# Kernel tuning notes

Hardware: AMD Instinct MI355X
Metric: run time of the kernel (lower is better)

The kernel has to match this reference:

```python
import jax, jax.numpy as jnp
import numpy as np

EPS = 1e-5


def _create_scalars(x0, x, N, basis, v):
    # x0: [b,NT,3], x/v: [b,NT,ND,3], N: [b,NT], basis: [b,Nb,3]
    b, NT, ND, _ = x.shape
    v0 = jnp.mean(v, axis=2)                       # [b,NT,3]
    v = v - v0[:, :, None, :]
    feats = []
    # local_N normalization (log scaling)
    Nn = jnp.log1p(N.astype(x.dtype))
    feats.append(jnp.broadcast_to(Nn[:, :, None, None], (b, NT, ND, 1)))
    x0n = jnp.linalg.norm(x0, axis=-1, keepdims=True) + EPS   # [b,NT,1]
    feats.append(jnp.broadcast_to(x0n[:, :, None, :], (b, NT, ND, 1)))
    x0u = x0 / x0n
    x0b = jnp.einsum('bid,bjd->bij', x0u, basis)              # [b,NT,Nb]
    feats.append(jnp.broadcast_to(x0b[:, :, None, :], (b, NT, ND, x0b.shape[-1])))
    v0n = jnp.linalg.norm(v0, axis=-1, keepdims=True) + EPS
    feats.append(jnp.broadcast_to(v0n[:, :, None, :], (b, NT, ND, 1)))
    v0u = v0 / v0n
    v0b = jnp.einsum('bid,bjd->bij', v0u, basis)
    feats.append(jnp.broadcast_to(v0b[:, :, None, :], (b, NT, ND, v0b.shape[-1])))
    x0v0 = jnp.einsum('bid,bid->bi', x0u, v0u)                # [b,NT]
    feats.append(jnp.broadcast_to(x0v0[:, :, None, None], (b, NT, ND, 1)))
    xn = jnp.linalg.norm(x, axis=-1, keepdims=True) + EPS     # [b,NT,ND,1]
    feats.append(xn)
    xu = x / xn
    feats.append(jnp.einsum('bijd,bkd->bijk', xu, basis))     # [b,NT,ND,Nb]
    vn = jnp.linalg.norm(v, axis=-1, keepdims=True) + EPS
    feats.append(vn)
    vu = v / vn
    feats.append(jnp.einsum('bijd,bkd->bijk', vu, basis))
    feats.append(jnp.einsum('bijd,bijd->bij', xu, vu)[..., None])
    return jnp.concatenate(feats, axis=-1)                    # [b,NT,ND,19]


def setup_inputs() -> dict:
    key = jax.random.key(0)
    ks = jax.random.split(key, 12)
    b, NT, ND, Nb = 4, 1024, 128, 3
    k_in, H, L = 19, 256, 128
    s0 = 1.0 / np.sqrt(k_in)
    s1 = 1.0 / np.sqrt(H)
    return {
        'x0': jax.random.normal(ks[0], (b, NT, 3), jnp.float32),
        'x': jax.random.normal(ks[1], (b, NT, ND, 3), jnp.float32),
        'N': jax.random.randint(ks[2], (b, NT), 1, 1000),
        'basis': jax.random.normal(ks[3], (b, Nb, 3), jnp.float32),
        'v': jax.random.normal(ks[4], (b, NT, ND, 3), jnp.float32),
        'W0': jax.random.normal(ks[5], (k_in, H), jnp.float32) * s0,
        'b0': jnp.zeros((H,), jnp.float32),
        'W1': jax.random.normal(ks[6], (H, H), jnp.float32) * s1,
        'b1': jnp.zeros((H,), jnp.float32),
        'W2': jax.random.normal(ks[7], (H, L), jnp.float32) * s1,
        'b2': jnp.zeros((L,), jnp.float32),
    }


def reference(x0, x, N, basis, v, W0, b0, W1, b1, W2, b2):
    s = _create_scalars(x0, x, N, basis, v)            # [b,NT,ND,19]
    h = jax.nn.leaky_relu(s @ W0 + b0)                 # layer 0 MLP
    h = jnp.mean(h, axis=2)                            # pool over N_DM -> [b,NT,H]
    h = jax.nn.leaky_relu(h @ W1 + b1)                 # layer 1
    return h @ W2 + b2                                 # layer 2 -> [b,NT,Nlatent]
```

## Files before the change

### kernel.cpp

```cpp
#include <hip/hip_runtime.h>
#include <math.h>

#define EPSF 1e-5f
constexpr int NT  = 1024;
constexpr int ND  = 128;
constexpr int KIN = 19;
constexpr int H   = 256;
constexpr int L   = 128;

typedef __attribute__((ext_vector_type(8))) short short8;
typedef __attribute__((ext_vector_type(4))) float f32x4;

static __device__ inline unsigned cvt_pk_bf16(float lo, float hi) {
    unsigned r;
    asm("v_cvt_pk_bf16_f32 %0, %1, %2" : "=v"(r) : "v"(lo), "v"(hi));
    return r;
}

__global__ __launch_bounds__(256) void k_fused(
    const float* __restrict__ x0, const float* __restrict__ x,
    const int*   __restrict__ Nv, const float* __restrict__ basis,
    const float* __restrict__ v,  const float* __restrict__ W0,
    const float* __restrict__ b0, float* __restrict__ hm_out)
{
    const int tid  = threadIdx.x;
    const int lane = tid & 63;
    const int w    = tid >> 6;
    const int g2   = blockIdx.x * 2;

    __shared__ __align__(16) ushort featb[2 * 512 * 8];
    __shared__ float psh[2][2][3];

    {
        const int sub  = tid >> 7;
        const int d    = tid & 127;
        const int g    = g2 + sub;
        const int bidx = g >> 10;

        const float* xp = x + (size_t)g * (ND * 3);
        const float* vp = v + (size_t)g * (ND * 3);
        const float vx = vp[d*3+0], vy = vp[d*3+1], vz = vp[d*3+2];
        const float xx = xp[d*3+0], xy = xp[d*3+1], xz = xp[d*3+2];

        float sx = vx, sy = vy, sz = vz;
        #pragma unroll
        for (int m = 1; m < 64; m <<= 1) {
            sx += __shfl_xor(sx, m, 64);
            sy += __shfl_xor(sy, m, 64);
            sz += __shfl_xor(sz, m, 64);
        }
        if (lane == 0) {
            psh[sub][w & 1][0] = sx;
            psh[sub][w & 1][1] = sy;
            psh[sub][w & 1][2] = sz;
        }
        __syncthreads();
        const float invd = 1.0f / (float)ND;
        const float v0x = (psh[sub][0][0] + psh[sub][1][0]) * invd;
        const float v0y = (psh[sub][0][1] + psh[sub][1][1]) * invd;
        const float v0z = (psh[sub][0][2] + psh[sub][1][2]) * invd;

        const float* bs = basis + bidx * 9;
        const float b0c = bs[0], b1c = bs[1], b2c = bs[2];
        const float b3c = bs[3], b4c = bs[4], b5c = bs[5];
        const float b6c = bs[6], b7c = bs[7], b8c = bs[8];

        unsigned u0, u1, u2, u3, u4;
        {
            const float ax = x0[g*3+0], ay = x0[g*3+1], az = x0[g*3+2];
            const float x0n = sqrtf(ax*ax + ay*ay + az*az) + EPSF;
            const float v0n = sqrtf(v0x*v0x + v0y*v0y + v0z*v0z) + EPSF;
            const float ix  = 1.f / x0n, iv0 = 1.f / v0n;
            u0 = cvt_pk_bf16(log1pf((float)Nv[g]), x0n);
            u1 = cvt_pk_bf16((ax*b0c + ay*b1c + az*b2c) * ix,
                             (ax*b3c + ay*b4c + az*b5c) * ix);
            u2 = cvt_pk_bf16((ax*b6c + ay*b7c + az*b8c) * ix, v0n);
            u3 = cvt_pk_bf16((v0x*b0c + v0y*b1c + v0z*b2c) * iv0,
                             (v0x*b3c + v0y*b4c + v0z*b5c) * iv0);
            u4 = cvt_pk_bf16((v0x*b6c + v0y*b7c + v0z*b8c) * iv0,
                             (ax*v0x + ay*v0y + az*v0z) * ix * iv0);
        }
        unsigned u5, u6, u7, u8, u9;
        {
            const float cx = vx - v0x, cy = vy - v0y, cz = vz - v0z;
            const float xn = sqrtf(xx*xx + xy*xy + xz*xz) + EPSF;
            const float vn = sqrtf(cx*cx + cy*cy + cz*cz) + EPSF;
            const float ixn = 1.f/xn, ivn = 1.f/vn;
            u5 = cvt_pk_bf16(xn, (xx*b0c + xy*b1c + xz*b2c) * ixn);
            u6 = cvt_pk_bf16((xx*b3c + xy*b4c + xz*b5c) * ixn,
                             (xx*b6c + xy*b7c + xz*b8c) * ixn);
            u7 = cvt_pk_bf16(vn, (cx*b0c + cy*b1c + cz*b2c) * ivn);
            u8 = cvt_pk_bf16((cx*b3c + cy*b4c + cz*b5c) * ivn,
                             (cx*b6c + cy*b7c + cz*b8c) * ivn);
            u9 = cvt_pk_bf16((xx*cx + xy*cy + xz*cz) * ixn * ivn, 1.0f);
        }

        const int mt  = d >> 4;
        const int r16 = d & 15;
        uint4* base = reinterpret_cast<uint4*>(
            &featb[((sub << 9) + (mt << 6) + r16) * 8]);
        base[0]  = uint4{u0, u1, u2, u3};
        base[16] = uint4{u4, u5, u6, u7};
        base[32] = uint4{u8, u9, 0u, 0u};
        base[48] = uint4{0u, 0u, 0u, 0u};
    }
    __syncthreads();

    short8 bfrag[4];
    {
        const int col16 = lane & 15;
        const int kb    = lane >> 4;
        #pragma unroll
        for (int nt = 0; nt < 4; ++nt) {
            const int col = w * 64 + nt * 16 + col16;
            uint4 pk;
            #pragma unroll
            for (int jj = 0; jj < 4; ++jj) {
                const int k0 = kb * 8 + 2*jj;
                const int k1 = k0 + 1;
                const float a = (k0 < KIN) ? W0[k0 * H + col]
                               : ((k0 == KIN) ? b0[col] : 0.f);
                const float b = (k1 < KIN) ? W0[k1 * H + col]
                               : ((k1 == KIN) ? b0[col] : 0.f);
                (&pk.x)[jj] = cvt_pk_bf16(a, b);
            }
            bfrag[nt] = *reinterpret_cast<short8*>(&pk);
        }
    }

    const f32x4 zc = {0.f, 0.f, 0.f, 0.f};
    const float invd = 1.0f / (float)ND;

    float a00 = 0.f, a01 = 0.f, a02 = 0.f, a03 = 0.f;
    float a10 = 0.f, a11 = 0.f, a12 = 0.f, a13 = 0.f;

    #pragma unroll 2
    for (int mt = 0; mt < 8; ++mt) {
        const short8 af0 = *reinterpret_cast<const short8*>(
            &featb[((mt << 6) + lane) * 8]);
        const short8 af1 = *reinterpret_cast<const short8*>(
            &featb[((512 + (mt << 6) + lane)) * 8]);
        {
            f32x4 d0 = __builtin_amdgcn_mfma_f32_16x16x32_bf16(af0, bfrag[0], zc, 0, 0, 0);
            f32x4 d1 = __builtin_amdgcn_mfma_f32_16x16x32_bf16(af1, bfrag[0], zc, 0, 0, 0);
            #pragma unroll
            for (int r = 0; r < 4; ++r) {
                a00 = fmaf(0.505f, d0[r], fmaf(0.495f, fabsf(d0[r]), a00));
                a10 = fmaf(0.505f, d1[r], fmaf(0.495f, fabsf(d1[r]), a10));
            }
        }
        {
            f32x4 d0 = __builtin_amdgcn_mfma_f32_16x16x32_bf16(af0, bfrag[1], zc, 0, 0, 0);
            f32x4 d1 = __builtin_amdgcn_mfma_f32_16x16x32_bf16(af1, bfrag[1], zc, 0, 0, 0);
            #pragma unroll
            for (int r = 0; r < 4; ++r) {
                a01 = fmaf(0.505f, d0[r], fmaf(0.495f, fabsf(d0[r]), a01));
                a11 = fmaf(0.505f, d1[r], fmaf(0.495f, fabsf(d1[r]), a11));
            }
        }
        {
            f32x4 d0 = __builtin_amdgcn_mfma_f32_16x16x32_bf16(af0, bfrag[2], zc, 0, 0, 0);
            f32x4 d1 = __builtin_amdgcn_mfma_f32_16x16x32_bf16(af1, bfrag[2], zc, 0, 0, 0);
            #pragma unroll
            for (int r = 0; r < 4; ++r) {
                a02 = fmaf(0.505f, d0[r], fmaf(0.495f, fabsf(d0[r]), a02));
                a12 = fmaf(0.505f, d1[r], fmaf(0.495f, fabsf(d1[r]), a12));
            }
        }
        {
            f32x4 d0 = __builtin_amdgcn_mfma_f32_16x16x32_bf16(af0, bfrag[3], zc, 0, 0, 0);
            f32x4 d1 = __builtin_amdgcn_mfma_f32_16x16x32_bf16(af1, bfrag[3], zc, 0, 0, 0);
            #pragma unroll
            for (int r = 0; r < 4; ++r) {
                a03 = fmaf(0.505f, d0[r], fmaf(0.495f, fabsf(d0[r]), a03));
                a13 = fmaf(0.505f, d1[r], fmaf(0.495f, fabsf(d1[r]), a13));
            }
        }
    }

    {
        float sv0[4] = {a00, a01, a02, a03};
        float sv1[4] = {a10, a11, a12, a13};
        #pragma unroll
        for (int nt = 0; nt < 4; ++nt) {
            float s4 = sv0[nt];
            s4 += __shfl_xor(s4, 16, 64);
            s4 += __shfl_xor(s4, 32, 64);
            float s5 = sv1[nt];
            s5 += __shfl_xor(s5, 16, 64);
            s5 += __shfl_xor(s5, 32, 64);
            if (lane < 16) {
                hm_out[(size_t)(g2 + 0) * H + w * 64 + nt * 16 + lane] = s4 * invd;
                hm_out[(size_t)(g2 + 1) * H + w * 64 + nt * 16 + lane] = s5 * invd;
            }
        }
    }
}

__global__ __launch_bounds__(256) void k_l12(
    const float* __restrict__ hm, const float* __restrict__ W1,
    const float* __restrict__ b1, const float* __restrict__ W2,
    const float* __restrict__ b2, float* __restrict__ out)
{
    const int tb  = blockIdx.x * 8;
    const int tid = threadIdx.x;
    __shared__ float hs[8][H];
    __shared__ float h1[8][H];

    {
        const float4* src = reinterpret_cast<const float4*>(hm + (size_t)tb * H);
        float4* dst = reinterpret_cast<float4*>(&hs[0][0]);
        #pragma unroll
        for (int i = 0; i < 2; ++i) dst[tid + i*256] = src[tid + i*256];
    }
    __syncthreads();

    {
        float acc[8];
        const float bb = b1[tid];
        #pragma unroll
        for (int t = 0; t < 8; ++t) acc[t] = bb;
        for (int k = 0; k < H; ++k) {
            const float w = W1[(size_t)k * H + tid];
            #pragma unroll
            for (int t = 0; t < 8; ++t) acc[t] = fmaf(hs[t][k], w, acc[t]);
        }
        #pragma unroll
        for (int t = 0; t < 8; ++t) {
            float a = acc[t];
            h1[t][tid] = (a > 0.f) ? a : 0.01f * a;
        }
    }
    __syncthreads();

    {
        const int n  = tid & 127;
        const int t0 = (tid >> 7) * 4;
        float acc[4];
        const float bb = b2[n];
        #pragma unroll
        for (int t = 0; t < 4; ++t) acc[t] = bb;
        for (int k = 0; k < H; ++k) {
            const float w = W2[(size_t)k * L + n];
            #pragma unroll
            for (int t = 0; t < 4; ++t) acc[t] = fmaf(h1[t0 + t][k], w, acc[t]);
        }
        #pragma unroll
        for (int t = 0; t < 4; ++t)
            out[(size_t)(tb + t0 + t) * L + n] = acc[t];
    }
}

extern "C" void kernel_launch(void* const* d_in, const int* in_sizes, int n_in,
                              void* d_out, int out_size, void* d_ws, size_t ws_size,
                              hipStream_t stream) {
    const float* x0    = (const float*)d_in[0];
    const float* x     = (const float*)d_in[1];
    const int*   Nv    = (const int*)  d_in[2];
    const float* basis = (const float*)d_in[3];
    const float* v     = (const float*)d_in[4];
    const float* W0    = (const float*)d_in[5];
    const float* b0    = (const float*)d_in[6];
    const float* W1    = (const float*)d_in[7];
    const float* b1    = (const float*)d_in[8];
    const float* W2    = (const float*)d_in[9];
    const float* b2    = (const float*)d_in[10];
    float* out = (float*)d_out;
    float* hm  = (float*)d_ws;

    hipLaunchKernelGGL(k_fused, dim3(4 * NT / 2), dim3(256), 0, stream,
                       x0, x, Nv, basis, v, W0, b0, hm);
    hipLaunchKernelGGL(k_l12, dim3(4 * NT / 8), dim3(256), 0, stream,
                       hm, W1, b1, W2, b2, out);
}
```

Before: 48.39 us.

## Process four groups per block with register prefetch of next x/v tile

Each block of the fused layer-0 kernel now handles four particle groups in two passes instead of two groups in one. The W0/b0 bf16 fragments and basis values are loaded once per block, which amortises their cost. The next pass's x and v values are loaded into registers before the current pass's feature build and MFMA work, so those global loads can overlap with compute. The grid is halved, which lowers parallelism and occupancy slack, and the block now runs more synchronisation points in sequence.

```diff
diff --git a/kernel.cpp b/kernel.cpp
--- a/kernel.cpp
+++ b/kernel.cpp
@@ -26,21 +26,66 @@
     const int tid  = threadIdx.x;
     const int lane = tid & 63;
     const int w    = tid >> 6;
-    const int g2   = blockIdx.x * 2;
+    const int sub  = tid >> 7;
+    const int d    = tid & 127;
+    const int gbase = blockIdx.x * 4;
+    const int bidx  = blockIdx.x >> 8;
 
     __shared__ __align__(16) ushort featb[2 * 512 * 8];
     __shared__ float psh[2][2][3];
 
-    {
-        const int sub  = tid >> 7;
-        const int d    = tid & 127;
-        const int g    = g2 + sub;
-        const int bidx = g >> 10;
-
-        const float* xp = x + (size_t)g * (ND * 3);
-        const float* vp = v + (size_t)g * (ND * 3);
-        const float vx = vp[d*3+0], vy = vp[d*3+1], vz = vp[d*3+2];
-        const float xx = xp[d*3+0], xy = xp[d*3+1], xz = xp[d*3+2];
+    const float* bs = basis + bidx * 9;
+    const float b0c = bs[0], b1c = bs[1], b2c = bs[2];
+    const float b3c = bs[3], b4c = bs[4], b5c = bs[5];
+    const float b6c = bs[6], b7c = bs[7], b8c = bs[8];
+
+    short8 bfrag[4];
+    {
+        const int col16 = lane & 15;
+        const int kb    = lane >> 4;
+        #pragma unroll
+        for (int nt = 0; nt < 4; ++nt) {
+            const int col = w * 64 + nt * 16 + col16;
+            uint4 pk;
+            #pragma unroll
+            for (int jj = 0; jj < 4; ++jj) {
+                const int k0 = kb * 8 + 2*jj;
+                const int k1 = k0 + 1;
+                const float a = (k0 < KIN) ? W0[k0 * H + col]
+                               : ((k0 == KIN) ? b0[col] : 0.f);
+                const float b = (k1 < KIN) ? W0[k1 * H + col]
+                               : ((k1 == KIN) ? b0[col] : 0.f);
+                (&pk.x)[jj] = cvt_pk_bf16(a, b);
+            }
+            bfrag[nt] = *reinterpret_cast<short8*>(&pk);
+        }
+    }
+
+    float xx, xy, xz, vx, vy, vz;
+    {
+        const int g = gbase + sub;
+        const float* xp = x + (size_t)g * (ND * 3) + d * 3;
+        const float* vp = v + (size_t)g * (ND * 3) + d * 3;
+        xx = xp[0]; xy = xp[1]; xz = xp[2];
+        vx = vp[0]; vy = vp[1]; vz = vp[2];
+    }
+
+    const f32x4 zc = {0.f, 0.f, 0.f, 0.f};
+    const float invd = 1.0f / (float)ND;
+
+    #pragma unroll
+    for (int p = 0; p < 2; ++p) {
+        const int gp2 = gbase + p * 2;
+        const int g   = gp2 + sub;
+
+        float nxx = 0.f, nxy = 0.f, nxz = 0.f, nvx = 0.f, nvy = 0.f, nvz = 0.f;
+        if (p == 0) {
+            const int gn = gbase + 2 + sub;
+            const float* xp = x + (size_t)gn * (ND * 3) + d * 3;
+            const float* vp = v + (size_t)gn * (ND * 3) + d * 3;
+            nxx = xp[0]; nxy = xp[1]; nxz = xp[2];
+            nvx = vp[0]; nvy = vp[1]; nvz = vp[2];
+        }
 
         float sx = vx, sy = vy, sz = vz;
         #pragma unroll
@@ -55,15 +100,9 @@
             psh[sub][w & 1][2] = sz;
         }
         __syncthreads();
-        const float invd = 1.0f / (float)ND;
         const float v0x = (psh[sub][0][0] + psh[sub][1][0]) * invd;
         const float v0y = (psh[sub][0][1] + psh[sub][1][1]) * invd;
         const float v0z = (psh[sub][0][2] + psh[sub][1][2]) * invd;
-
-        const float* bs = basis + bidx * 9;
-        const float b0c = bs[0], b1c = bs[1], b2c = bs[2];
-        const float b3c = bs[3], b4c = bs[4], b5c = bs[5];
-        const float b6c = bs[6], b7c = bs[7], b8c = bs[8];
 
         unsigned u0, u1, u2, u3, u4;
         {
@@ -102,98 +141,76 @@
         base[0]  = uint4{u0, u1, u2, u3};
         base[16] = uint4{u4, u5, u6, u7};
         base[32] = uint4{u8, u9, 0u, 0u};
-        base[48] = uint4{0u, 0u, 0u, 0u};
-    }
-    __syncthreads();
-
-    short8 bfrag[4];
-    {
-        const int col16 = lane & 15;
-        const int kb    = lane >> 4;
-        #pragma unroll
-        for (int nt = 0; nt < 4; ++nt) {
-            const int col = w * 64 + nt * 16 + col16;
-            uint4 pk;
-            #pragma unroll
-            for (int jj = 0; jj < 4; ++jj) {
-                const int k0 = kb * 8 + 2*jj;
-                const int k1 = k0 + 1;
-                const float a = (k0 < KIN) ? W0[k0 * H + col]
-                               : ((k0 == KIN) ? b0[col] : 0.f);
-                const float b = (k1 < KIN) ? W0[k1 * H + col]
-                               : ((k1 == KIN) ? b0[col] : 0.f);
-                (&pk.x)[jj] = cvt_pk_bf16(a, b);
-            }
-            bfrag[nt] = *reinterpret_cast<short8*>(&pk);
-        }
-    }
-
-    const f32x4 zc = {0.f, 0.f, 0.f, 0.f};
-    const float invd = 1.0f / (float)ND;
-
-    float a00 = 0.f, a01 = 0.f, a02 = 0.f, a03 = 0.f;
-    float a10 = 0.f, a11 = 0.f, a12 = 0.f, a13 = 0.f;
-
-    #pragma unroll 2
-    for (int mt = 0; mt < 8; ++mt) {
-        const short8 af0 = *reinterpret_cast<const short8*>(
-            &featb[((mt << 6) + lane) * 8]);
-        const short8 af1 = *reinterpret_cast<const short8*>(
-            &featb[((512 + (mt << 6) + lane)) * 8]);
+        if (p == 0) base[48] = uint4{0u, 0u, 0u, 0u};
+        __syncthreads();
+
+        float a00 = 0.f, a01 = 0.f, a02 = 0.f, a03 = 0.f;
+        float a10 = 0.f, a11 = 0.f, a12 = 0.f, a13 = 0.f;
+
+        #pragma unroll 2
+        for (int m2 = 0; m2 < 8; ++m2) {
+            const short8 af0 = *reinterpret_cast<const short8*>(
+                &featb[((m2 << 6) + lane) * 8]);
+            const short8 af1 = *reinterpret_cast<const short8*>(
+                &featb[(512 + (m2 << 6) + lane) * 8]);
+            {
+                f32x4 d0 = __builtin_amdgcn_mfma_f32_16x16x32_bf16(af0, bfrag[0], zc, 0, 0, 0);
+                f32x4 d1 = __builtin_amdgcn_mfma_f32_16x16x32_bf16(af1, bfrag[0], zc, 0, 0, 0);
+                #pragma unroll
+                for (int r = 0; r < 4; ++r) {
+                    a00 = fmaf(0.505f, d0[r], fmaf(0.495f, fabsf(d0[r]), a00));
+                    a10 = fmaf(0.505f, d1[r], fmaf(0.495f, fabsf(d1[r]), a10));
+                }
+            }
+            {
+                f32x4 d0 = __builtin_amdgcn_mfma_f32_16x16x32_bf16(af0, bfrag[1], zc, 0, 0, 0);
+                f32x4 d1 = __builtin_amdgcn_mfma_f32_16x16x32_bf16(af1, bfrag[1], zc, 0, 0, 0);
+                #pragma unroll
+                for (int r = 0; r < 4; ++r) {
+                    a01 = fmaf(0.505f, d0[r], fmaf(0.495f, fabsf(d0[r]), a01));
+                    a11 = fmaf(0.505f, d1[r], fmaf(0.495f, fabsf(d1[r]), a11));
+                }
+            }
+            {
+                f32x4 d0 = __builtin_amdgcn_mfma_f32_16x16x32_bf16(af0, bfrag[2], zc, 0, 0, 0);
+                f32x4 d1 = __builtin_amdgcn_mfma_f32_16x16x32_bf16(af1, bfrag[2], zc, 0, 0, 0);
+                #pragma unroll
+                for (int r = 0; r < 4; ++r) {
+                    a02 = fmaf(0.505f, d0[r], fmaf(0.495f, fabsf(d0[r]), a02));
+                    a12 = fmaf(0.505f, d1[r], fmaf(0.495f, fabsf(d1[r]), a12));
+                }
+            }
+            {
+                f32x4 d0 = __builtin_amdgcn_mfma_f32_16x16x32_bf16(af0, bfrag[3], zc, 0, 0, 0);
+                f32x4 d1 = __builtin_amdgcn_mfma_f32_16x16x32_bf16(af1, bfrag[3], zc, 0, 0, 0);
+                #pragma unroll
+                for (int r = 0; r < 4; ++r) {
+                    a03 = fmaf(0.505f, d0[r], fmaf(0.495f, fabsf(d0[r]), a03));
+                    a13 = fmaf(0.505f, d1[r], fmaf(0.495f, fabsf(d1[r]), a13));
+                }
+            }
+        }
+
         {
-            f32x4 d0 = __builtin_amdgcn_mfma_f32_16x16x32_bf16(af0, bfrag[0], zc, 0, 0, 0);
-            f32x4 d1 = __builtin_amdgcn_mfma_f32_16x16x32_bf16(af1, bfrag[0], zc, 0, 0, 0);
-            #pragma unroll
-            for (int r = 0; r < 4; ++r) {
-                a00 = fmaf(0.505f, d0[r], fmaf(0.495f, fabsf(d0[r]), a00));
-                a10 = fmaf(0.505f, d1[r], fmaf(0.495f, fabsf(d1[r]), a10));
-            }
-        }
-        {
-            f32x4 d0 = __builtin_amdgcn_mfma_f32_16x16x32_bf16(af0, bfrag[1], zc, 0, 0, 0);
-            f32x4 d1 = __builtin_amdgcn_mfma_f32_16x16x32_bf16(af1, bfrag[1], zc, 0, 0, 0);
-            #pragma unroll
-            for (int r = 0; r < 4; ++r) {
-                a01 = fmaf(0.505f, d0[r], fmaf(0.495f, fabsf(d0[r]), a01));
-                a11 = fmaf(0.505f, d1[r], fmaf(0.495f, fabsf(d1[r]), a11));
-            }
-        }
-        {
-            f32x4 d0 = __builtin_amdgcn_mfma_f32_16x16x32_bf16(af0, bfrag[2], zc, 0, 0, 0);
-            f32x4 d1 = __builtin_amdgcn_mfma_f32_16x16x32_bf16(af1, bfrag[2], zc, 0, 0, 0);
-            #pragma unroll
-            for (int r = 0; r < 4; ++r) {
-                a02 = fmaf(0.505f, d0[r], fmaf(0.495f, fabsf(d0[r]), a02));
-                a12 = fmaf(0.505f, d1[r], fmaf(0.495f, fabsf(d1[r]), a12));
-            }
-        }
-        {
-            f32x4 d0 = __builtin_amdgcn_mfma_f32_16x16x32_bf16(af0, bfrag[3], zc, 0, 0, 0);
-            f32x4 d1 = __builtin_amdgcn_mfma_f32_16x16x32_bf16(af1, bfrag[3], zc, 0, 0, 0);
-            #pragma unroll
-            for (int r = 0; r < 4; ++r) {
-                a03 = fmaf(0.505f, d0[r], fmaf(0.495f, fabsf(d0[r]), a03));
-                a13 = fmaf(0.505f, d1[r], fmaf(0.495f, fabsf(d1[r]), a13));
-            }
-        }
-    }
-
-    {
-        float sv0[4] = {a00, a01, a02, a03};
-        float sv1[4] = {a10, a11, a12, a13};
-        #pragma unroll
-        for (int nt = 0; nt < 4; ++nt) {
-            float s4 = sv0[nt];
-            s4 += __shfl_xor(s4, 16, 64);
-            s4 += __shfl_xor(s4, 32, 64);
-            float s5 = sv1[nt];
-            s5 += __shfl_xor(s5, 16, 64);
-            s5 += __shfl_xor(s5, 32, 64);
-            if (lane < 16) {
-                hm_out[(size_t)(g2 + 0) * H + w * 64 + nt * 16 + lane] = s4 * invd;
-                hm_out[(size_t)(g2 + 1) * H + w * 64 + nt * 16 + lane] = s5 * invd;
-            }
-        }
+            float sv0[4] = {a00, a01, a02, a03};
+            float sv1[4] = {a10, a11, a12, a13};
+            #pragma unroll
+            for (int nt = 0; nt < 4; ++nt) {
+                float s4 = sv0[nt];
+                s4 += __shfl_xor(s4, 16, 64);
+                s4 += __shfl_xor(s4, 32, 64);
+                float s5 = sv1[nt];
+                s5 += __shfl_xor(s5, 16, 64);
+                s5 += __shfl_xor(s5, 32, 64);
+                if (lane < 16) {
+                    hm_out[(size_t)(gp2 + 0) * H + w * 64 + nt * 16 + lane] = s4 * invd;
+                    hm_out[(size_t)(gp2 + 1) * H + w * 64 + nt * 16 + lane] = s5 * invd;
+                }
+            }
+        }
+
+        xx = nxx; xy = nxy; xz = nxz;
+        vx = nvx; vy = nvy; vz = nvz;
     }
 }
 
@@ -268,7 +285,7 @@
     float* out = (float*)d_out;
     float* hm  = (float*)d_ws;
 
-    hipLaunchKernelGGL(k_fused, dim3(4 * NT / 2), dim3(256), 0, stream,
+    hipLaunchKernelGGL(k_fused, dim3(4 * NT / 4), dim3(256), 0, stream,
                        x0, x, Nv, basis, v, W0, b0, hm);
     hipLaunchKernelGGL(k_l12, dim3(4 * NT / 8), dim3(256), 0, stream,
                        hm, W1, b1, W2, b2, out);
```

After: 50.64 us. 1.05x slower.

## Split per-particle mean-velocity precompute into separate kernel to drop block barrier

Applied to the files above, without the earlier changes.

Adds a k_pre kernel that computes each group's mean velocity and the per-group scalar features (log N, x0 norm, basis projections, v0 terms) and stores them as two float4 per group in workspace. The fused kernel then loads these values instead of doing a cross-wave shuffle reduction plus a __syncthreads before building features. This removes the mid-kernel barrier and the redundant per-thread group-scalar math. In exchange it adds a third launch, and v is read twice from global memory.

```diff
diff --git a/kernel.cpp b/kernel.cpp
--- a/kernel.cpp
+++ b/kernel.cpp
@@ -17,11 +17,57 @@
     return r;
 }
 
+__global__ __launch_bounds__(256) void k_pre(
+    const float* __restrict__ x0, const int* __restrict__ Nv,
+    const float* __restrict__ basis, const float* __restrict__ v,
+    float4* __restrict__ pre)
+{
+    const int tid  = threadIdx.x;
+    const int lane = tid & 63;
+    const int w    = tid >> 6;
+    const int g    = blockIdx.x * 4 + w;
+    const int bidx = g >> 10;
+
+    const float* vp = v + (size_t)g * (ND * 3);
+    const float vx0 = vp[lane*3+0],      vy0 = vp[lane*3+1],      vz0 = vp[lane*3+2];
+    const float vx1 = vp[(lane+64)*3+0], vy1 = vp[(lane+64)*3+1], vz1 = vp[(lane+64)*3+2];
+
+    float sx = vx0 + vx1, sy = vy0 + vy1, sz = vz0 + vz1;
+    #pragma unroll
+    for (int m = 1; m < 64; m <<= 1) {
+        sx += __shfl_xor(sx, m, 64);
+        sy += __shfl_xor(sy, m, 64);
+        sz += __shfl_xor(sz, m, 64);
+    }
+    const float invd = 1.0f / (float)ND;
+    const float v0x = sx * invd, v0y = sy * invd, v0z = sz * invd;
+
+    const float* bs = basis + bidx * 9;
+    const float ax = x0[g*3+0], ay = x0[g*3+1], az = x0[g*3+2];
+    const float x0n = sqrtf(ax*ax + ay*ay + az*az) + EPSF;
+    const float v0n = sqrtf(v0x*v0x + v0y*v0y + v0z*v0z) + EPSF;
+    const float ix  = 1.f / x0n, iv0 = 1.f / v0n;
+    const unsigned u0 = cvt_pk_bf16(log1pf((float)Nv[g]), x0n);
+    const unsigned u1 = cvt_pk_bf16((ax*bs[0] + ay*bs[1] + az*bs[2]) * ix,
+                                    (ax*bs[3] + ay*bs[4] + az*bs[5]) * ix);
+    const unsigned u2 = cvt_pk_bf16((ax*bs[6] + ay*bs[7] + az*bs[8]) * ix, v0n);
+    const unsigned u3 = cvt_pk_bf16((v0x*bs[0] + v0y*bs[1] + v0z*bs[2]) * iv0,
+                                    (v0x*bs[3] + v0y*bs[4] + v0z*bs[5]) * iv0);
+    const unsigned u4 = cvt_pk_bf16((v0x*bs[6] + v0y*bs[7] + v0z*bs[8]) * iv0,
+                                    (ax*v0x + ay*v0y + az*v0z) * ix * iv0);
+
+    if (lane == 0) {
+        pre[g*2 + 0] = float4{v0x, v0y, v0z, __uint_as_float(u0)};
+        pre[g*2 + 1] = float4{__uint_as_float(u1), __uint_as_float(u2),
+                              __uint_as_float(u3), __uint_as_float(u4)};
+    }
+}
+
 __global__ __launch_bounds__(256) void k_fused(
-    const float* __restrict__ x0, const float* __restrict__ x,
-    const int*   __restrict__ Nv, const float* __restrict__ basis,
-    const float* __restrict__ v,  const float* __restrict__ W0,
-    const float* __restrict__ b0, float* __restrict__ hm_out)
+    const float* __restrict__ x, const float* __restrict__ v,
+    const float4* __restrict__ pre, const float* __restrict__ basis,
+    const float* __restrict__ W0, const float* __restrict__ b0,
+    float* __restrict__ hm_out)
 {
     const int tid  = threadIdx.x;
     const int lane = tid & 63;
@@ -29,7 +75,6 @@
     const int g2   = blockIdx.x * 2;
 
     __shared__ __align__(16) ushort featb[2 * 512 * 8];
-    __shared__ float psh[2][2][3];
 
     {
         const int sub  = tid >> 7;
@@ -37,63 +82,36 @@
         const int g    = g2 + sub;
         const int bidx = g >> 10;
 
-        const float* xp = x + (size_t)g * (ND * 3);
-        const float* vp = v + (size_t)g * (ND * 3);
-        const float vx = vp[d*3+0], vy = vp[d*3+1], vz = vp[d*3+2];
-        const float xx = xp[d*3+0], xy = xp[d*3+1], xz = xp[d*3+2];
-
-        float sx = vx, sy = vy, sz = vz;
-        #pragma unroll
-        for (int m = 1; m < 64; m <<= 1) {
-            sx += __shfl_xor(sx, m, 64);
-            sy += __shfl_xor(sy, m, 64);
-            sz += __shfl_xor(sz, m, 64);
-        }
-        if (lane == 0) {
-            psh[sub][w & 1][0] = sx;
-            psh[sub][w & 1][1] = sy;
-            psh[sub][w & 1][2] = sz;
-        }
-        __syncthreads();
-        const float invd = 1.0f / (float)ND;
-        const float v0x = (psh[sub][0][0] + psh[sub][1][0]) * invd;
-        const float v0y = (psh[sub][0][1] + psh[sub][1][1]) * invd;
-        const float v0z = (psh[sub][0][2] + psh[sub][1][2]) * invd;
+        const float* xp = x + (size_t)g * (ND * 3) + d * 3;
+        const float* vp = v + (size_t)g * (ND * 3) + d * 3;
+        const float xx = xp[0], xy = xp[1], xz = xp[2];
+        const float vx = vp[0], vy = vp[1], vz = vp[2];
+
+        const float4 p0 = pre[g*2 + 0];
+        const float4 p1 = pre[g*2 + 1];
+        const float v0x = p0.x, v0y = p0.y, v0z = p0.z;
+        const unsigned u0 = __float_as_uint(p0.w);
+        const unsigned u1 = __float_as_uint(p1.x);
+        const unsigned u2 = __float_as_uint(p1.y);
+        const unsigned u3 = __float_as_uint(p1.z);
+        const unsigned u4 = __float_as_uint(p1.w);
 
         const float* bs = basis + bidx * 9;
         const float b0c = bs[0], b1c = bs[1], b2c = bs[2];
         const float b3c = bs[3], b4c = bs[4], b5c = bs[5];
         const float b6c = bs[6], b7c = bs[7], b8c = bs[8];
 
-        unsigned u0, u1, u2, u3, u4;
-        {
-            const float ax = x0[g*3+0], ay = x0[g*3+1], az = x0[g*3+2];
-            const float x0n = sqrtf(ax*ax + ay*ay + az*az) + EPSF;
-            const float v0n = sqrtf(v0x*v0x + v0y*v0y + v0z*v0z) + EPSF;
-            const float ix  = 1.f / x0n, iv0 = 1.f / v0n;
-            u0 = cvt_pk_bf16(log1pf((float)Nv[g]), x0n);
-            u1 = cvt_pk_bf16((ax*b0c + ay*b1c + az*b2c) * ix,
-                             (ax*b3c + ay*b4c + az*b5c) * ix);
-            u2 = cvt_pk_bf16((ax*b6c + ay*b7c + az*b8c) * ix, v0n);
-            u3 = cvt_pk_bf16((v0x*b0c + v0y*b1c + v0z*b2c) * iv0,
-                             (v0x*b3c + v0y*b4c + v0z*b5c) * iv0);
-            u4 = cvt_pk_bf16((v0x*b6c + v0y*b7c + v0z*b8c) * iv0,
-                             (ax*v0x + ay*v0y + az*v0z) * ix * iv0);
-        }
-        unsigned u5, u6, u7, u8, u9;
-        {
-            const float cx = vx - v0x, cy = vy - v0y, cz = vz - v0z;
-            const float xn = sqrtf(xx*xx + xy*xy + xz*xz) + EPSF;
-            const float vn = sqrtf(cx*cx + cy*cy + cz*cz) + EPSF;
-            const float ixn = 1.f/xn, ivn = 1.f/vn;
-            u5 = cvt_pk_bf16(xn, (xx*b0c + xy*b1c + xz*b2c) * ixn);
-            u6 = cvt_pk_bf16((xx*b3c + xy*b4c + xz*b5c) * ixn,
-                             (xx*b6c + xy*b7c + xz*b8c) * ixn);
-            u7 = cvt_pk_bf16(vn, (cx*b0c + cy*b1c + cz*b2c) * ivn);
-            u8 = cvt_pk_bf16((cx*b3c + cy*b4c + cz*b5c) * ivn,
-                             (cx*b6c + cy*b7c + cz*b8c) * ivn);
-            u9 = cvt_pk_bf16((xx*cx + xy*cy + xz*cz) * ixn * ivn, 1.0f);
-        }
+        const float cx = vx - v0x, cy = vy - v0y, cz = vz - v0z;
+        const float xn = sqrtf(xx*xx + xy*xy + xz*xz) + EPSF;
+        const float vn = sqrtf(cx*cx + cy*cy + cz*cz) + EPSF;
+        const float ixn = 1.f/xn, ivn = 1.f/vn;
+        const unsigned u5 = cvt_pk_bf16(xn, (xx*b0c + xy*b1c + xz*b2c) * ixn);
+        const unsigned u6 = cvt_pk_bf16((xx*b3c + xy*b4c + xz*b5c) * ixn,
+                                        (xx*b6c + xy*b7c + xz*b8c) * ixn);
+        const unsigned u7 = cvt_pk_bf16(vn, (cx*b0c + cy*b1c + cz*b2c) * ivn);
+        const unsigned u8 = cvt_pk_bf16((cx*b3c + cy*b4c + cz*b5c) * ivn,
+                                        (cx*b6c + cy*b7c + cz*b8c) * ivn);
+        const unsigned u9 = cvt_pk_bf16((xx*cx + xy*cy + xz*cz) * ixn * ivn, 1.0f);
 
         const int mt  = d >> 4;
         const int r16 = d & 15;
@@ -139,7 +157,7 @@
         const short8 af0 = *reinterpret_cast<const short8*>(
             &featb[((mt << 6) + lane) * 8]);
         const short8 af1 = *reinterpret_cast<const short8*>(
-            &featb[((512 + (mt << 6) + lane)) * 8]);
+            &featb[(512 + (mt << 6) + lane) * 8]);
         {
             f32x4 d0 = __builtin_amdgcn_mfma_f32_16x16x32_bf16(af0, bfrag[0], zc, 0, 0, 0);
             f32x4 d1 = __builtin_amdgcn_mfma_f32_16x16x32_bf16(af1, bfrag[0], zc, 0, 0, 0);
@@ -266,10 +284,14 @@
     const float* W2    = (const float*)d_in[9];
     const float* b2    = (const float*)d_in[10];
     float* out = (float*)d_out;
-    float* hm  = (float*)d_ws;
-
+
+    float*  hm  = (float*)d_ws;
+    float4* pre = (float4*)((char*)d_ws + (size_t)4*1024*1024);
+
+    hipLaunchKernelGGL(k_pre, dim3(4 * NT / 4), dim3(256), 0, stream,
+                       x0, Nv, basis, v, pre);
     hipLaunchKernelGGL(k_fused, dim3(4 * NT / 2), dim3(256), 0, stream,
-                       x0, x, Nv, basis, v, W0, b0, hm);
+                       x, v, pre, basis, W0, b0, hm);
     hipLaunchKernelGGL(k_l12, dim3(4 * NT / 8), dim3(256), 0, stream,
                        hm, W1, b1, W2, b2, out);
 }
```

Result: slower. 52.08 us (+7.6%).
